# Kernel tuning notes

Hardware: AMD Instinct MI355X
Metric: run time of the kernel (lower is better)

The kernel has to match this reference:

```python
import jax, jax.numpy as jnp
import numpy as np

EPS = 1e-6
NEG = -1e9
W = 8          # chunk_size
H_MA = 4       # monotonic heads
H_CA = 1       # chunkwise heads
ADIM = 1024
SHARP = 1.0    # sharpening_factor
SCALE = float(np.sqrt(ADIM))


def moving_sum(x, back, forward):
    # windowed sum over last axis, window = back+forward+1 (small, fixed)
    K = x.shape[-1]
    pad = [(0, 0)] * (x.ndim - 1) + [(back, forward)]
    xp = jnp.pad(x, pad)
    out = xp[..., 0:K]
    for d in range(1, back + forward + 1):
        out = out + xp[..., d:d + K]
    return out


def exclusive_cumsum(x):
    z = jnp.zeros(x.shape[:-1] + (1,), x.dtype)
    return jnp.cumsum(jnp.concatenate([z, x[..., :-1]], axis=-1), axis=-1)


def setup_inputs():
    key0 = jax.random.key(0)
    ks = jax.random.split(key0, 12)
    B, K, Q, D = 16, 2000, 256, 1024
    nrm = lambda k, shp, s=1.0: jax.random.normal(k, shp, jnp.float32) * s
    aw_prev = jnp.zeros((B, H_MA, 1, K), jnp.float32).at[..., 0].set(1.0)
    return {
        'key': nrm(ks[0], (B, K, D)),
        'value': nrm(ks[1], (B, K, D)),
        'query': nrm(ks[2], (B, Q, D)),
        'mask': jnp.ones((B, Q, K), jnp.int32),
        'aw_prev': aw_prev,
        'Wk_ma': nrm(ks[3], (D, ADIM), 0.02), 'bk_ma': jnp.zeros((ADIM,), jnp.float32),
        'Wq_ma': nrm(ks[4], (D, ADIM), 0.02), 'bq_ma': jnp.zeros((ADIM,), jnp.float32),
        'r': jnp.full((1,), -4.0, jnp.float32),
        'Wk_ca': nrm(ks[5], (D, ADIM), 0.02), 'bk_ca': jnp.zeros((ADIM,), jnp.float32),
        'Wq_ca': nrm(ks[6], (D, ADIM), 0.02), 'bq_ca': jnp.zeros((ADIM,), jnp.float32),
        'Wv': nrm(ks[7], (D, ADIM), 0.02), 'bv': jnp.zeros((ADIM,), jnp.float32),
        'Wo': nrm(ks[8], (ADIM, D), 0.02), 'bo': jnp.zeros((D,), jnp.float32),
    }


def reference(key, value, query, mask, aw_prev,
              Wk_ma, bk_ma, Wq_ma, bq_ma, r,
              Wk_ca, bk_ca, Wq_ca, bq_ca, Wv, bv, Wo, bo):
    B, K, D = key.shape
    Q = query.shape[1]
    dk_ma = ADIM // H_MA
    H_tot = H_MA * H_CA
    dk_ca = ADIM // H_tot
    m = (mask[:, None] != 0)  # [B,1,Q,K]

    # ---- monotonic energy: [B,H_ma,Q,K]
    k_ma = (key @ Wk_ma + bk_ma).reshape(B, K, H_MA, dk_ma)
    q_ma = (query @ Wq_ma + bq_ma).reshape(B, Q, H_MA, dk_ma)
    e_ma = jnp.einsum('bqhd,bkhd->bhqk', q_ma, k_ma) / SCALE + r[0]
    e_ma = jnp.where(m, e_ma, NEG)

    # ---- monotonic alignment alpha (parallel training mode)
    p = jax.nn.sigmoid(e_ma)                                  # [B,H,Q,K]
    log1mp = jnp.log(jnp.clip(1.0 - p, EPS, 1.0))
    cp = jnp.exp(exclusive_cumsum(log1mp))                    # safe_cumprod(1-p)

    def step(aw, pc):
        p_i, cp_i = pc                                        # [B,H,K]
        denom = jnp.clip(cp_i, EPS, 1.0)
        aw_new = p_i * cp_i * jnp.cumsum(aw / denom, axis=-1)
        return aw_new, aw_new

    xs = (p.transpose(2, 0, 1, 3), cp.transpose(2, 0, 1, 3))  # [Q,B,H,K]
    _, alphas = jax.lax.scan(step, aw_prev[:, :, 0], xs)
    alpha = alphas.transpose(1, 2, 0, 3)                      # [B,H_ma,Q,K]

    # ---- chunk energy: [B,H_ma*H_ca,Q,K]
    k_ca = (key @ Wk_ca + bk_ca).reshape(B, K, H_tot, dk_ca)
    q_ca = (query @ Wq_ca + bq_ca).reshape(B, Q, H_tot, dk_ca)
    e_ca = jnp.einsum('bqhd,bkhd->bhqk', q_ca, k_ca) / SCALE
    e_ca = jnp.where(m, e_ca, NEG)

    # ---- soft chunkwise attention (moving-sum windowed softmax)
    u = e_ca.reshape(B, H_MA, H_CA, Q, K)
    a5 = alpha[:, :, None] * SHARP                            # [B,H_ma,1,Q,K]
    u = u - jnp.max(u, axis=-1, keepdims=True)
    se = jnp.clip(jnp.exp(u), 1e-5, None)
    denom = moving_sum(se, W - 1, 0)
    beta = se * moving_sum(a5 / denom, 0, W - 1)
    beta = beta.reshape(B, H_tot, Q, K)

    # ---- context + output projection
    v = (value @ Wv + bv).reshape(B, K, H_tot, dk_ca)
    cv = jnp.einsum('bhqk,bkhd->bqhd', beta, v).reshape(B, Q, ADIM)
    return cv @ Wo + bo
```

## Files before the change

### kernel.cpp

```cpp
#include <hip/hip_runtime.h>


typedef __bf16 bf16x8_t __attribute__((ext_vector_type(8)));
typedef float f32x4_t __attribute__((ext_vector_type(4)));
typedef unsigned short ushort8_t __attribute__((ext_vector_type(8)));
typedef unsigned short ushort4_t __attribute__((ext_vector_type(4)));
typedef unsigned int uint4_t __attribute__((ext_vector_type(4)));

__device__ __forceinline__ unsigned short f2bf(float x) {
  unsigned int u = __builtin_bit_cast(unsigned int, x);
  u += 0x7fffu + ((u >> 16) & 1u);
  return (unsigned short)(u >> 16);
}
__device__ __forceinline__ float bf2f(unsigned short h) {
  unsigned int u = ((unsigned int)h) << 16;
  return __builtin_bit_cast(float, u);
}

__device__ __forceinline__ void gld16(const unsigned short* g, unsigned short* l) {
  __builtin_amdgcn_global_load_lds(
      (const __attribute__((address_space(1))) void*)g,
      (__attribute__((address_space(3))) void*)l, 16, 0, 0);
}

__device__ __forceinline__ float wave_incl_scan(float x) {
  float v = x;
  int mv;
#define DPP_ADD(ctrl, rmask, bctrl)                                           \
  mv = __builtin_amdgcn_update_dpp(0, __builtin_bit_cast(int, v), ctrl,       \
                                   rmask, 0xf, bctrl);                        \
  v += __builtin_bit_cast(float, mv);
  DPP_ADD(0x111, 0xf, true);
  DPP_ADD(0x112, 0xf, true);
  DPP_ADD(0x114, 0xf, true);
  DPP_ADD(0x118, 0xf, true);
  DPP_ADD(0x142, 0xa, false);
  DPP_ADD(0x143, 0xc, false);
#undef DPP_ADD
  return v;
}

__device__ __forceinline__ float wave_max_bcast(float x) {
  const float NI = -__builtin_inff();
  float v = x;
  int mv;
#define DPP_MAX(ctrl, rmask)                                                  \
  mv = __builtin_amdgcn_update_dpp(__builtin_bit_cast(int, NI),               \
                                   __builtin_bit_cast(int, v), ctrl, rmask,   \
                                   0xf, false);                               \
  v = fmaxf(v, __builtin_bit_cast(float, mv));
  DPP_MAX(0x111, 0xf) DPP_MAX(0x112, 0xf) DPP_MAX(0x114, 0xf)
  DPP_MAX(0x118, 0xf) DPP_MAX(0x142, 0xa) DPP_MAX(0x143, 0xc)
#undef DPP_MAX
  int r = __builtin_amdgcn_readlane(__builtin_bit_cast(int, v), 63);
  return __builtin_bit_cast(float, r);
}

#define WSHR1(dst, src)                                                       \
  {                                                                           \
    int _t = __builtin_amdgcn_update_dpp(0, __builtin_bit_cast(int, src),     \
                                         0x138, 0xf, 0xf, true);              \
    dst = __builtin_bit_cast(float, _t);                                      \
  }
#define WSHL1(dst, src)                                                       \
  {                                                                           \
    int _t = __builtin_amdgcn_update_dpp(0, __builtin_bit_cast(int, src),     \
                                         0x130, 0xf, 0xf, true);              \
    dst = __builtin_bit_cast(float, _t);                                      \
  }

__device__ __forceinline__ void gemm_bt_tile(
    const unsigned short* __restrict__ A, long lda,
    const unsigned short* __restrict__ B, long ldb,
    int Kd, unsigned short* lA, unsigned short* lB, f32x4_t acc[4][4]) {
  const int tid = threadIdx.x;
  const int lane = tid & 63;
  const int wid = tid >> 6;
  const int wm = wid >> 1, wn = wid & 1;
  const int lr = lane & 15, quad = lane >> 4;
  const int srow = wid * 32 + (lane >> 3);
  const int scol = ((lane & 7) ^ (lane >> 3)) * 8;
  const int rs = lr & 7;
  for (int ks = 0; ks < Kd; ks += 64) {
    __syncthreads();
    const unsigned short* Ag = A + (long)srow * lda + ks + scol;
    const unsigned short* Bg = B + (long)srow * ldb + ks + scol;
#pragma unroll
    for (int r = 0; r < 4; ++r) {
      gld16(Ag + (long)(r * 8) * lda, lA + (wid * 32 + r * 8) * 64);
      gld16(Bg + (long)(r * 8) * ldb, lB + (wid * 32 + r * 8) * 64);
    }
    __syncthreads();
#pragma unroll
    for (int kk = 0; kk < 2; ++kk) {
      bf16x8_t afr[4], bfr[4];
#pragma unroll
      for (int i = 0; i < 4; ++i)
        afr[i] = *(const bf16x8_t*)(lA + (wm * 64 + i * 16 + lr) * 64 +
                                    (((kk * 4 + quad) ^ rs) << 3));
#pragma unroll
      for (int j = 0; j < 4; ++j)
        bfr[j] = *(const bf16x8_t*)(lB + (wn * 64 + j * 16 + lr) * 64 +
                                    (((kk * 4 + quad) ^ rs) << 3));
#pragma unroll
      for (int i = 0; i < 4; ++i)
#pragma unroll
        for (int j = 0; j < 4; ++j)
          acc[i][j] = __builtin_amdgcn_mfma_f32_16x16x32_bf16(afr[i], bfr[j], acc[i][j], 0, 0, 0);
    }
  }
}

#define EPILOGUE_IDX()                                          \
  const int tid = threadIdx.x, lane = tid & 63, wid = tid >> 6; \
  const int wm = wid >> 1, wn = wid & 1, lr = lane & 15, quad = lane >> 4;

#define ACC_INIT()                              \
  f32x4_t acc[4][4];                            \
  _Pragma("unroll") for (int i = 0; i < 4; ++i) \
  _Pragma("unroll") for (int j = 0; j < 4; ++j) \
  _Pragma("unroll") for (int r = 0; r < 4; ++r) acc[i][j][r] = 0.f;

__device__ __forceinline__ void epi_stash(float* lT, f32x4_t (&acc)[4][4],
                                          int i, int wm, int wn, int lr, int quad) {
#pragma unroll
  for (int j = 0; j < 4; ++j) {
    int lcol = wn * 64 + j * 16 + lr;
#pragma unroll
    for (int r = 0; r < 4; ++r) {
      int lrow = wm * 16 + quad * 4 + r;
      lT[lrow * 128 + (((lcol >> 2) ^ (lrow & 7)) << 2) + (lcol & 3)] = acc[i][j][r];
    }
  }
}
__device__ __forceinline__ f32x4_t epi_read(const float* lT, int rloc, int col4) {
  return *(const f32x4_t*)&lT[rloc * 128 + ((col4 ^ (rloc & 7)) << 2)];
}

__global__ __launch_bounds__(256) void k_proj(const unsigned short* __restrict__ A,
                                              const unsigned short* __restrict__ Wt,
                                              const float* __restrict__ bias,
                                              unsigned short* __restrict__ C) {
  __shared__ __attribute__((aligned(16))) char smem[32768];
  unsigned short* lA = (unsigned short*)smem;
  unsigned short* lB = (unsigned short*)(smem + 16384);
  float* lT = (float*)smem;
  ACC_INIT();
  int flat = blockIdx.x;
  int mb = (flat >> 6) * 8 + (flat & 7);
  int nb = (flat >> 3) & 7;
  const unsigned short* Ab = A + (long)mb * 128 * 1024;
  const unsigned short* Bb = Wt + (long)nb * 128 * 1024;
  gemm_bt_tile(Ab, 1024, Bb, 1024, 1024, lA, lB, acc);
  EPILOGUE_IDX();
  (void)lane;
  long mbase = (long)mb * 128;
  int nbase = nb * 128;
  const int rloc = tid >> 3, c7 = tid & 7;
#pragma unroll
  for (int i = 0; i < 4; ++i) {
    __syncthreads();
    epi_stash(lT, acc, i, wm, wn, lr, quad);
    __syncthreads();
    long mg = mbase + (rloc >> 4) * 64 + i * 16 + (rloc & 15);
    unsigned short* crow = C + mg * 1024 + nbase;
    const float* brow = bias + nbase;
#pragma unroll
    for (int m = 0; m < 4; ++m) {
      int col4 = c7 + 8 * m;
      f32x4_t v = epi_read(lT, rloc, col4);
      f32x4_t bv = *(const f32x4_t*)&brow[col4 * 4];
      ushort4_t o;
#pragma unroll
      for (int z = 0; z < 4; ++z) o[z] = f2bf(v[z] + bv[z]);
      *(ushort4_t*)(crow + col4 * 4) = o;
    }
  }
}

__global__ __launch_bounds__(256) void k_maskpack(const int* __restrict__ mask,
                                                  unsigned int* __restrict__ mw) {
  int lane = threadIdx.x & 63, wid = threadIdx.x >> 6;
  int row = blockIdx.x * 4 + wid;
  const int* mp = mask + (long)row * 2000;
  unsigned int* op = mw + (long)row * 64;
  for (int c = 0; c < 32; ++c) {
    int k = c * 64 + lane;
    int v = (k < 2000) ? mp[k] : 0;
    unsigned long long b = __ballot(v != 0);
    if (lane == 0) {
      op[c * 2] = (unsigned int)b;
      op[c * 2 + 1] = (unsigned int)(b >> 32);
    }
  }
}

__global__ __launch_bounds__(256) void k_escore(const unsigned short* __restrict__ qproj,
                                                const unsigned short* __restrict__ kproj,
                                                const unsigned int* __restrict__ maskw,
                                                const float* __restrict__ rptr,
                                                unsigned short* __restrict__ outp, int is_ma) {
  __shared__ __attribute__((aligned(16))) char smem[32768];
  unsigned short* lA = (unsigned short*)smem;
  unsigned short* lB = (unsigned short*)(smem + 16384);
  float* lT = (float*)smem;
  ACC_INIT();
  int bz = blockIdx.z, b = bz >> 2, h = bz & 3;
  int nrow0 = blockIdx.x * 128;
  const unsigned short* Ab = qproj + ((long)b * 256 + blockIdx.y * 128) * 1024 + h * 256;
  const unsigned short* Bb = kproj + ((long)b * 2048 + nrow0) * 1024 + h * 256;
  gemm_bt_tile(Ab, 1024, Bb, 1024, 256, lA, lB, acc);
  float rv = is_ma ? rptr[0] : 0.f;
  EPILOGUE_IDX();
  (void)lane;
  const int rloc = tid >> 3, c7 = tid & 7;
#pragma unroll
  for (int i = 0; i < 4; ++i) {
    __syncthreads();
    epi_stash(lT, acc, i, wm, wn, lr, quad);
    __syncthreads();
    int qg = blockIdx.y * 128 + (rloc >> 4) * 64 + i * 16 + (rloc & 15);
    uint4_t mw4 = *(const uint4_t*)(maskw + (((long)b * 256 + qg) << 6) + (nrow0 >> 5));
    unsigned short* orow = outp + ((long)bz * 256 + qg) * 2048 + nrow0;
#pragma unroll
    for (int m = 0; m < 4; ++m) {
      int col4 = c7 + 8 * m;
      f32x4_t v = epi_read(lT, rloc, col4);
      unsigned int bits = (mw4[m] >> (4 * c7)) & 0xFu;
      ushort4_t o;
#pragma unroll
      for (int z = 0; z < 4; ++z) {
        float e = v[z] * 0.03125f;
        bool valid = (bits >> z) & 1u;
        float ov;
        if (is_ma)
          ov = valid ? (1.f / (1.f + __expf(-(e + rv)))) : 0.f;
        else
          ov = valid ? e : -1e9f;
        o[z] = f2bf(ov);
      }
      *(ushort4_t*)(orow + col4 * 4) = o;
    }
  }
}

__global__ __launch_bounds__(256) void k_cp(const unsigned short* __restrict__ p,
                                            unsigned short* __restrict__ cp) {
  __shared__ float wsum[4];
  long base = (long)blockIdx.x * 2048;
  int tid = threadIdx.x, lane = tid & 63, wid = tid >> 6;
  ushort8_t p8 = *(const ushort8_t*)(p + base + tid * 8);
  float lex[8], s1 = 0.f;
#pragma unroll
  for (int i = 0; i < 8; ++i) {
    float om = fminf(fmaxf(1.f - bf2f((unsigned short)p8[i]), 1e-6f), 1.f);
    lex[i] = s1;
    s1 += __logf(om);
  }
  float incl = wave_incl_scan(s1);
  if (lane == 63) wsum[wid] = incl;
  __syncthreads();
  float off = incl - s1;
  if (wid > 0) off += wsum[0];
  if (wid > 1) off += wsum[1];
  if (wid > 2) off += wsum[2];
  ushort8_t o;
#pragma unroll
  for (int i = 0; i < 8; ++i) o[i] = f2bf(__expf(off + lex[i]));
  *(ushort8_t*)(cp + base + tid * 8) = o;
}

__global__ __launch_bounds__(256) void k_scan(const unsigned short* __restrict__ p,
                                              const unsigned short* cp,
                                              const float* __restrict__ awp,
                                              unsigned short* alpha) {
  __shared__ unsigned short lsp[2][2][2048];
  __shared__ unsigned short lsc[2][2][2048];
  __shared__ float wsum[2][4];
  int bh = blockIdx.x;
  int tid = threadIdx.x, lane = tid & 63, w = tid >> 6;
  long base = (long)bh * 256 * 2048;
  float aw[8];
  const float* ap = awp + (long)bh * 2000;
#pragma unroll
  for (int i = 0; i < 8; ++i) {
    int k = tid * 8 + i;
    aw[i] = (k < 2000) ? ap[k] : 0.f;
  }
  const unsigned short* pg = p + base;
  const unsigned short* cg = cp + base;
  unsigned short* ag = alpha + base;
  const int sa = w >> 1;
  const int sr = w & 1;
  const unsigned short* sbase = (sa ? cg : pg) + (long)sr * 2048 + lane * 8;
#define STAGE(c, b)                                                           \
  {                                                                           \
    const unsigned short* _src = sbase + (long)(c) * 2 * 2048;                \
    unsigned short* _dst = sa ? &lsc[b][sr][0] : &lsp[b][sr][0];              \
    _Pragma("unroll") for (int _q = 0; _q < 4; ++_q)                          \
        gld16(_src + _q * 512, _dst + _q * 512);                              \
  }
  STAGE(0, 0);
  asm volatile("s_waitcnt vmcnt(0)" ::: "memory");
  __builtin_amdgcn_s_barrier();
  asm volatile("" ::: "memory");
  for (int c = 0; c < 128; ++c) {
    const int b = c & 1;
    if (c < 127) STAGE(c + 1, b ^ 1);
#pragma unroll
    for (int cr = 0; cr < 2; ++cr) {
      const int q = c * 2 + cr;
      ushort8_t p8 = *(const ushort8_t*)&lsp[b][cr][tid * 8];
      ushort8_t c8 = *(const ushort8_t*)&lsc[b][cr][tid * 8];
      float pc[8], rd[8];
#pragma unroll
      for (int i = 0; i < 8; ++i) {
        float pv = bf2f((unsigned short)p8[i]);
        float cv = bf2f((unsigned short)c8[i]);
        pc[i] = pv * cv;
        rd[i] = __builtin_amdgcn_rcpf(fminf(fmaxf(cv, 1e-6f), 1.f));
      }
      float t[8], s1 = 0.f;
#pragma unroll
      for (int i = 0; i < 8; ++i) {
        s1 = fmaf(aw[i], rd[i], s1);
        t[i] = s1;
      }
      float incl = wave_incl_scan(s1);
      if (lane == 63) wsum[q & 1][w] = incl;
      asm volatile("s_waitcnt lgkmcnt(0)" ::: "memory");
      __builtin_amdgcn_s_barrier();
      asm volatile("" ::: "memory");
      float off = incl - s1;
      if (w > 0) off += wsum[q & 1][0];
      if (w > 1) off += wsum[q & 1][1];
      if (w > 2) off += wsum[q & 1][2];
      ushort8_t o;
#pragma unroll
      for (int i = 0; i < 8; ++i) {
        aw[i] = pc[i] * (t[i] + off);
        o[i] = f2bf(aw[i]);
      }
      *(ushort8_t*)(ag + (long)q * 2048 + tid * 8) = o;
    }
    asm volatile("s_waitcnt vmcnt(2)" ::: "memory");
    __builtin_amdgcn_s_barrier();
    asm volatile("" ::: "memory");
  }
#undef STAGE
}

__global__ __launch_bounds__(256) void k_beta(unsigned short* eca,
                                              const unsigned short* __restrict__ alpha) {
  __shared__ float red[4];
  __shared__ float edgeB[4][8];
  __shared__ float edgeF[4][8];
  long base = (long)blockIdx.x * 2048 + threadIdx.x * 8;
  int tid = threadIdx.x, lane = tid & 63, wid = tid >> 6;
  (void)tid;
  ushort8_t u8 = *(const ushort8_t*)(eca + base);
  ushort8_t a8 = *(const ushort8_t*)(alpha + base);
  float u[8], a[8];
#pragma unroll
  for (int i = 0; i < 8; ++i) {
    u[i] = bf2f((unsigned short)u8[i]);
    a[i] = bf2f((unsigned short)a8[i]);
  }
  float m = u[0];
#pragma unroll
  for (int i = 1; i < 8; ++i) m = fmaxf(m, u[i]);
  m = wave_max_bcast(m);
  if (lane == 0) red[wid] = m;
  __syncthreads();
  m = fmaxf(fmaxf(red[0], red[1]), fmaxf(red[2], red[3]));
  float se[8], lp[8];
  float s = 0.f;
#pragma unroll
  for (int i = 0; i < 8; ++i) {
    se[i] = fmaxf(__expf(u[i] - m), 1e-5f);
    s += se[i];
    lp[i] = s;
  }
  float plp[8];
#pragma unroll
  for (int i = 0; i < 8; ++i) WSHR1(plp[i], lp[i]);
  if (lane == 63) {
#pragma unroll
    for (int i = 0; i < 8; ++i) edgeB[wid][i] = lp[i];
  }
  __syncthreads();
  if (lane == 0 && wid > 0) {
#pragma unroll
    for (int i = 0; i < 8; ++i) plp[i] = edgeB[wid - 1][i];
  }
  float sra[8], lf[8];
  s = 0.f;
#pragma unroll
  for (int i = 0; i < 8; ++i) {
    float msb = lp[i] + plp[7] - plp[i];
    sra[i] = a[i] * __builtin_amdgcn_rcpf(msb);
    s += sra[i];
    lf[i] = s;
  }
  float nlf[8];
#pragma unroll
  for (int i = 0; i < 8; ++i) WSHL1(nlf[i], lf[i]);
  if (lane == 0) {
#pragma unroll
    for (int i = 0; i < 8; ++i) edgeF[wid][i] = lf[i];
  }
  __syncthreads();
  if (lane == 63 && wid < 3) {
#pragma unroll
    for (int i = 0; i < 8; ++i) nlf[i] = edgeF[wid + 1][i];
  }
  ushort8_t o;
#pragma unroll
  for (int i = 0; i < 8; ++i) {
    float own = lf[7] - (i ? lf[i - 1] : 0.f);
    float nxt = i ? nlf[i - 1] : 0.f;
    o[i] = f2bf(se[i] * (own + nxt));
  }
  *(ushort8_t*)(eca + base) = o;
}

__global__ __launch_bounds__(256) void k_build_vT(const unsigned short* __restrict__ v,
                                                  unsigned short* __restrict__ vT) {
  __shared__ unsigned short t[64][68];
  int bz = blockIdx.z, b = bz >> 2, h = bz & 3;
  int k0 = blockIdx.x * 64, d0 = blockIdx.y * 64;
  int tx = threadIdx.x & 63, tg = threadIdx.x >> 6;
#pragma unroll
  for (int i = 0; i < 16; ++i) {
    int kk = tg * 16 + i;
    t[kk][tx] = v[((long)(b * 2048 + k0 + kk)) * 1024 + h * 256 + d0 + tx];
  }
  __syncthreads();
#pragma unroll
  for (int i = 0; i < 16; ++i) {
    int dd = tg * 16 + i;
    vT[((long)bz * 256 + d0 + dd) * 2048 + k0 + tx] = t[tx][dd];
  }
}

__global__ __launch_bounds__(256) void k_cv(const unsigned short* __restrict__ beta,
                                            const unsigned short* __restrict__ vT,
                                            unsigned short* __restrict__ cv) {
  __shared__ __attribute__((aligned(16))) char smem[32768];
  unsigned short* lA = (unsigned short*)smem;
  unsigned short* lB = (unsigned short*)(smem + 16384);
  float* lT = (float*)smem;
  ACC_INIT();
  int bz = blockIdx.z, b = bz >> 2, h = bz & 3;
  const unsigned short* Ab = beta + (long)bz * 256 * 2048 + (long)blockIdx.y * 128 * 2048;
  const unsigned short* Bb = vT + (long)bz * 256 * 2048 + (long)blockIdx.x * 128 * 2048;
  gemm_bt_tile(Ab, 2048, Bb, 2048, 2048, lA, lB, acc);
  EPILOGUE_IDX();
  (void)lane;
  const int rloc = tid >> 3, c7 = tid & 7;
#pragma unroll
  for (int i = 0; i < 4; ++i) {
    __syncthreads();
    epi_stash(lT, acc, i, wm, wn, lr, quad);
    __syncthreads();
    long mg = (long)b * 256 + blockIdx.y * 128 + (rloc >> 4) * 64 + i * 16 + (rloc & 15);
    unsigned short* crow = cv + mg * 1024 + h * 256 + blockIdx.x * 128;
#pragma unroll
    for (int m = 0; m < 4; ++m) {
      int col4 = c7 + 8 * m;
      f32x4_t v = epi_read(lT, rloc, col4);
      ushort4_t o;
#pragma unroll
      for (int z = 0; z < 4; ++z) o[z] = f2bf(v[z]);
      *(ushort4_t*)(crow + col4 * 4) = o;
    }
  }
}

__global__ __launch_bounds__(256) void k_out(const unsigned short* __restrict__ cv,
                                             const unsigned short* __restrict__ WoT,
                                             const float* __restrict__ bo,
                                             float* __restrict__ outp) {
  __shared__ __attribute__((aligned(16))) char smem[32768];
  unsigned short* lA = (unsigned short*)smem;
  unsigned short* lB = (unsigned short*)(smem + 16384);
  float* lT = (float*)smem;
  ACC_INIT();
  const unsigned short* Ab = cv + (long)blockIdx.y * 128 * 1024;
  const unsigned short* Bb = WoT + (long)blockIdx.x * 128 * 1024;
  gemm_bt_tile(Ab, 1024, Bb, 1024, 1024, lA, lB, acc);
  EPILOGUE_IDX();
  (void)lane;
  const int rloc = tid >> 3, c7 = tid & 7;
#pragma unroll
  for (int i = 0; i < 4; ++i) {
    __syncthreads();
    epi_stash(lT, acc, i, wm, wn, lr, quad);
    __syncthreads();
    long mg = (long)blockIdx.y * 128 + (rloc >> 4) * 64 + i * 16 + (rloc & 15);
    float* orow = outp + mg * 1024 + blockIdx.x * 128;
    const float* brow = bo + blockIdx.x * 128;
#pragma unroll
    for (int m = 0; m < 4; ++m) {
      int col4 = c7 + 8 * m;
      f32x4_t v = epi_read(lT, rloc, col4);
      f32x4_t bv = *(const f32x4_t*)&brow[col4 * 4];
      *(f32x4_t*)&orow[col4 * 4] = v + bv;
    }
  }
}

__global__ __launch_bounds__(256) void k_twT(const float* __restrict__ W,
                                             unsigned short* __restrict__ Wt) {
  __shared__ float t[32][33];
  int bx = blockIdx.x, by = blockIdx.y;
  int lx = threadIdx.x & 31, ly = threadIdx.x >> 5;
#pragma unroll
  for (int r = 0; r < 4; ++r)
    t[ly + 8 * r][lx] = W[((long)(by * 32 + ly + 8 * r)) * 1024 + bx * 32 + lx];
  __syncthreads();
#pragma unroll
  for (int r = 0; r < 4; ++r)
    Wt[((long)(bx * 32 + ly + 8 * r)) * 1024 + by * 32 + lx] = f2bf(t[lx][ly + 8 * r]);
}

__global__ __launch_bounds__(256) void k_cvt_pad(const float* __restrict__ src,
                                                 unsigned short* __restrict__ dst) {
  long idx = (long)blockIdx.x * 256 + threadIdx.x;
  int b = (int)(idx >> 18);
  int rem = (int)(idx & 262143);
  int row = rem >> 7;
  int c8 = rem & 127;
  ushort8_t o;
  if (row < 2000) {
    const float* sp = src + ((long)(b * 2000 + row)) * 1024 + c8 * 8;
    float4 f0 = *(const float4*)sp;
    float4 f1 = *(const float4*)(sp + 4);
    o[0] = f2bf(f0.x); o[1] = f2bf(f0.y); o[2] = f2bf(f0.z); o[3] = f2bf(f0.w);
    o[4] = f2bf(f1.x); o[5] = f2bf(f1.y); o[6] = f2bf(f1.z); o[7] = f2bf(f1.w);
  } else {
#pragma unroll
    for (int z = 0; z < 8; ++z) o[z] = 0;
  }
  *(ushort8_t*)(dst + idx * 8) = o;
}

__global__ __launch_bounds__(256) void k_cvt(const float* __restrict__ src,
                                             unsigned short* __restrict__ dst) {
  long idx = (long)blockIdx.x * 256 + threadIdx.x;
  const float* sp = src + idx * 8;
  float4 f0 = *(const float4*)sp;
  float4 f1 = *(const float4*)(sp + 4);
  ushort8_t o;
  o[0] = f2bf(f0.x); o[1] = f2bf(f0.y); o[2] = f2bf(f0.z); o[3] = f2bf(f0.w);
  o[4] = f2bf(f1.x); o[5] = f2bf(f1.y); o[6] = f2bf(f1.z); o[7] = f2bf(f1.w);
  *(ushort8_t*)(dst + idx * 8) = o;
}

extern "C" void kernel_launch(void* const* d_in, const int* in_sizes, int n_in,
                              void* d_out, int out_size, void* d_ws, size_t ws_size,
                              hipStream_t stream) {
  const float* key = (const float*)d_in[0];
  const float* value = (const float*)d_in[1];
  const float* query = (const float*)d_in[2];
  const int* mask = (const int*)d_in[3];
  const float* awp = (const float*)d_in[4];
  const float* Wk_ma = (const float*)d_in[5];
  const float* bk_ma = (const float*)d_in[6];
  const float* Wq_ma = (const float*)d_in[7];
  const float* bq_ma = (const float*)d_in[8];
  const float* rvec = (const float*)d_in[9];
  const float* Wk_ca = (const float*)d_in[10];
  const float* bk_ca = (const float*)d_in[11];
  const float* Wq_ca = (const float*)d_in[12];
  const float* bq_ca = (const float*)d_in[13];
  const float* Wv = (const float*)d_in[14];
  const float* bv = (const float*)d_in[15];
  const float* Wo = (const float*)d_in[16];
  const float* bo = (const float*)d_in[17];
  float* outp = (float*)d_out;
  (void)in_sizes; (void)n_in; (void)out_size;

  char* ws = (char*)d_ws;
  size_t off = 0;
  auto alloc = [&](size_t bytes) {
    void* pp = ws + off;
    off += (bytes + 255) & ~(size_t)255;
    return pp;
  };
  unsigned short* wt[6];
  for (int i = 0; i < 6; ++i) wt[i] = (unsigned short*)alloc(1024L * 1024 * 2);
  unsigned short* xbf = (unsigned short*)alloc(16L * 2048 * 1024 * 2);
  unsigned short* qbf = (unsigned short*)alloc(4096L * 1024 * 2);
  unsigned short* kproj = (unsigned short*)alloc(16L * 2048 * 1024 * 2);
  unsigned short* qproj = (unsigned short*)alloc(4096L * 1024 * 2);
  unsigned short* bufP = (unsigned short*)alloc(64L * 256 * 2048 * 2);
  unsigned short* bufA = (unsigned short*)alloc(64L * 256 * 2048 * 2);
  unsigned int* maskw = (unsigned int*)alloc(4096L * 64 * 4);
  if (ws_size < off) return;
  unsigned short* cv_bf = qbf;

  dim3 blk(256);
  k_twT<<<dim3(32, 32), blk, 0, stream>>>(Wk_ma, wt[0]);
  k_twT<<<dim3(32, 32), blk, 0, stream>>>(Wq_ma, wt[1]);
  k_twT<<<dim3(32, 32), blk, 0, stream>>>(Wk_ca, wt[2]);
  k_twT<<<dim3(32, 32), blk, 0, stream>>>(Wq_ca, wt[3]);
  k_twT<<<dim3(32, 32), blk, 0, stream>>>(Wv, wt[4]);
  k_twT<<<dim3(32, 32), blk, 0, stream>>>(Wo, wt[5]);
  k_maskpack<<<dim3(1024), blk, 0, stream>>>(mask, maskw);
  k_cvt_pad<<<dim3(16384), blk, 0, stream>>>(key, xbf);
  k_cvt<<<dim3(2048), blk, 0, stream>>>(query, qbf);
  k_proj<<<dim3(2048), blk, 0, stream>>>(xbf, wt[0], bk_ma, kproj);
  k_proj<<<dim3(256), blk, 0, stream>>>(qbf, wt[1], bq_ma, qproj);
  k_escore<<<dim3(16, 2, 64), blk, 0, stream>>>(qproj, kproj, maskw, rvec, bufP, 1);
  k_cp<<<dim3(16384), blk, 0, stream>>>(bufP, bufA);
  k_proj<<<dim3(2048), blk, 0, stream>>>(xbf, wt[2], bk_ca, kproj);
  k_proj<<<dim3(256), blk, 0, stream>>>(qbf, wt[3], bq_ca, qproj);
  k_scan<<<dim3(64), blk, 0, stream>>>(bufP, bufA, awp, bufA);
  k_escore<<<dim3(16, 2, 64), blk, 0, stream>>>(qproj, kproj, maskw, rvec, bufP, 0);
  k_beta<<<dim3(16384), blk, 0, stream>>>(bufP, bufA);
  k_cvt_pad<<<dim3(16384), blk, 0, stream>>>(value, xbf);
  k_proj<<<dim3(2048), blk, 0, stream>>>(xbf, wt[4], bv, kproj);
  k_build_vT<<<dim3(32, 4, 64), blk, 0, stream>>>(kproj, bufA);
  k_cv<<<dim3(2, 2, 64), blk, 0, stream>>>(bufP, bufA, cv_bf);
  k_out<<<dim3(8, 32), blk, 0, stream>>>(cv_bf, wt[5], bo, outp);
}
```

Measured before the change: 1.031 ms.

## Double-buffer GEMM LDS tiles and triple-buffer monotonic scan staging

The shared GEMM tile loop now uses two LDS buffers per operand, issuing the global-to-LDS loads for the next K step before computing on the current one, with explicit vmcnt waits and raw barriers in place of the two syncthreads per step. The monotonic alpha scan kernel moves from two to three staging buffers so loads run two chunks ahead. The aim is to hide global load latency behind MFMA and scan work. The cost is doubled GEMM shared memory (64KB per block), which may lower occupancy, plus reliance on hand-tuned vmcnt counts being correct.

```diff
diff --git a/kernel.cpp b/kernel.cpp
--- a/kernel.cpp
+++ b/kernel.cpp
@@ -69,10 +69,22 @@
     dst = __builtin_bit_cast(float, _t);                                      \
   }
 
+__device__ __forceinline__ void gemm_stage(const unsigned short* Ag, long lda,
+                                           const unsigned short* Bg, long ldb,
+                                           int wid, unsigned short* lA,
+                                           unsigned short* lB) {
+#pragma unroll
+  for (int r = 0; r < 4; ++r) {
+    gld16(Ag + (long)(r * 8) * lda, lA + (wid * 32 + r * 8) * 64);
+    gld16(Bg + (long)(r * 8) * ldb, lB + (wid * 32 + r * 8) * 64);
+  }
+}
+
 __device__ __forceinline__ void gemm_bt_tile(
     const unsigned short* __restrict__ A, long lda,
-    const unsigned short* __restrict__ B, long ldb,
-    int Kd, unsigned short* lA, unsigned short* lB, f32x4_t acc[4][4]) {
+    const unsigned short* __restrict__ B, long ldb, int Kd,
+    unsigned short* lA0, unsigned short* lB0,
+    unsigned short* lA1, unsigned short* lB1, f32x4_t acc[4][4]) {
   const int tid = threadIdx.x;
   const int lane = tid & 63;
   const int wid = tid >> 6;
@@ -81,26 +93,33 @@
   const int srow = wid * 32 + (lane >> 3);
   const int scol = ((lane & 7) ^ (lane >> 3)) * 8;
   const int rs = lr & 7;
-  for (int ks = 0; ks < Kd; ks += 64) {
-    __syncthreads();
-    const unsigned short* Ag = A + (long)srow * lda + ks + scol;
-    const unsigned short* Bg = B + (long)srow * ldb + ks + scol;
-#pragma unroll
-    for (int r = 0; r < 4; ++r) {
-      gld16(Ag + (long)(r * 8) * lda, lA + (wid * 32 + r * 8) * 64);
-      gld16(Bg + (long)(r * 8) * ldb, lB + (wid * 32 + r * 8) * 64);
-    }
-    __syncthreads();
+  const unsigned short* Ag = A + (long)srow * lda + scol;
+  const unsigned short* Bg = B + (long)srow * ldb + scol;
+  const int nt = Kd >> 6;
+  gemm_stage(Ag, lda, Bg, ldb, wid, lA0, lB0);
+  for (int t = 0; t < nt; ++t) {
+    unsigned short* cA = (t & 1) ? lA1 : lA0;
+    unsigned short* cB = (t & 1) ? lB1 : lB0;
+    if (t + 1 < nt) {
+      unsigned short* nA = (t & 1) ? lA0 : lA1;
+      unsigned short* nB = (t & 1) ? lB0 : lB1;
+      gemm_stage(Ag + (t + 1) * 64, lda, Bg + (t + 1) * 64, ldb, wid, nA, nB);
+      asm volatile("s_waitcnt vmcnt(8)" ::: "memory");
+    } else {
+      asm volatile("s_waitcnt vmcnt(0)" ::: "memory");
+    }
+    __builtin_amdgcn_s_barrier();
+    asm volatile("" ::: "memory");
 #pragma unroll
     for (int kk = 0; kk < 2; ++kk) {
       bf16x8_t afr[4], bfr[4];
 #pragma unroll
       for (int i = 0; i < 4; ++i)
-        afr[i] = *(const bf16x8_t*)(lA + (wm * 64 + i * 16 + lr) * 64 +
+        afr[i] = *(const bf16x8_t*)(cA + (wm * 64 + i * 16 + lr) * 64 +
                                     (((kk * 4 + quad) ^ rs) << 3));
 #pragma unroll
       for (int j = 0; j < 4; ++j)
-        bfr[j] = *(const bf16x8_t*)(lB + (wn * 64 + j * 16 + lr) * 64 +
+        bfr[j] = *(const bf16x8_t*)(cB + (wn * 64 + j * 16 + lr) * 64 +
                                     (((kk * 4 + quad) ^ rs) << 3));
 #pragma unroll
       for (int i = 0; i < 4; ++i)
@@ -108,6 +127,8 @@
         for (int j = 0; j < 4; ++j)
           acc[i][j] = __builtin_amdgcn_mfma_f32_16x16x32_bf16(afr[i], bfr[j], acc[i][j], 0, 0, 0);
     }
+    asm volatile("" ::: "memory");
+    __builtin_amdgcn_s_barrier();
   }
 }
 
@@ -121,6 +142,14 @@
   _Pragma("unroll") for (int j = 0; j < 4; ++j) \
   _Pragma("unroll") for (int r = 0; r < 4; ++r) acc[i][j][r] = 0.f;
 
+#define GEMM_SMEM()                                        \
+  __shared__ __attribute__((aligned(16))) char smem[65536]; \
+  unsigned short* lA0 = (unsigned short*)smem;             \
+  unsigned short* lB0 = (unsigned short*)(smem + 16384);   \
+  unsigned short* lA1 = (unsigned short*)(smem + 32768);   \
+  unsigned short* lB1 = (unsigned short*)(smem + 49152);   \
+  float* lT = (float*)smem;
+
 __device__ __forceinline__ void epi_stash(float* lT, f32x4_t (&acc)[4][4],
                                           int i, int wm, int wn, int lr, int quad) {
 #pragma unroll
@@ -141,17 +170,14 @@
                                               const unsigned short* __restrict__ Wt,
                                               const float* __restrict__ bias,
                                               unsigned short* __restrict__ C) {
-  __shared__ __attribute__((aligned(16))) char smem[32768];
-  unsigned short* lA = (unsigned short*)smem;
-  unsigned short* lB = (unsigned short*)(smem + 16384);
-  float* lT = (float*)smem;
+  GEMM_SMEM();
   ACC_INIT();
   int flat = blockIdx.x;
   int mb = (flat >> 6) * 8 + (flat & 7);
   int nb = (flat >> 3) & 7;
   const unsigned short* Ab = A + (long)mb * 128 * 1024;
   const unsigned short* Bb = Wt + (long)nb * 128 * 1024;
-  gemm_bt_tile(Ab, 1024, Bb, 1024, 1024, lA, lB, acc);
+  gemm_bt_tile(Ab, 1024, Bb, 1024, 1024, lA0, lB0, lA1, lB1, acc);
   EPILOGUE_IDX();
   (void)lane;
   long mbase = (long)mb * 128;
@@ -200,16 +226,13 @@
                                                 const unsigned int* __restrict__ maskw,
                                                 const float* __restrict__ rptr,
                                                 unsigned short* __restrict__ outp, int is_ma) {
-  __shared__ __attribute__((aligned(16))) char smem[32768];
-  unsigned short* lA = (unsigned short*)smem;
-  unsigned short* lB = (unsigned short*)(smem + 16384);
-  float* lT = (float*)smem;
+  GEMM_SMEM();
   ACC_INIT();
   int bz = blockIdx.z, b = bz >> 2, h = bz & 3;
   int nrow0 = blockIdx.x * 128;
   const unsigned short* Ab = qproj + ((long)b * 256 + blockIdx.y * 128) * 1024 + h * 256;
   const unsigned short* Bb = kproj + ((long)b * 2048 + nrow0) * 1024 + h * 256;
-  gemm_bt_tile(Ab, 1024, Bb, 1024, 256, lA, lB, acc);
+  gemm_bt_tile(Ab, 1024, Bb, 1024, 256, lA0, lB0, lA1, lB1, acc);
   float rv = is_ma ? rptr[0] : 0.f;
   EPILOGUE_IDX();
   (void)lane;
@@ -274,8 +297,8 @@
                                               const unsigned short* cp,
                                               const float* __restrict__ awp,
                                               unsigned short* alpha) {
-  __shared__ unsigned short lsp[2][2][2048];
-  __shared__ unsigned short lsc[2][2][2048];
+  __shared__ unsigned short lsp[3][2][2048];
+  __shared__ unsigned short lsc[3][2][2048];
   __shared__ float wsum[2][4];
   int bh = blockIdx.x;
   int tid = threadIdx.x, lane = tid & 63, w = tid >> 6;
@@ -301,12 +324,19 @@
         gld16(_src + _q * 512, _dst + _q * 512);                              \
   }
   STAGE(0, 0);
-  asm volatile("s_waitcnt vmcnt(0)" ::: "memory");
-  __builtin_amdgcn_s_barrier();
-  asm volatile("" ::: "memory");
+  STAGE(1, 1);
   for (int c = 0; c < 128; ++c) {
-    const int b = c & 1;
-    if (c < 127) STAGE(c + 1, b ^ 1);
+    const int b = c % 3;
+    if (c + 2 < 128) {
+      STAGE(c + 2, (c + 2) % 3);
+      asm volatile("s_waitcnt vmcnt(8)" ::: "memory");
+    } else if (c + 1 < 128) {
+      asm volatile("s_waitcnt vmcnt(4)" ::: "memory");
+    } else {
+      asm volatile("s_waitcnt vmcnt(0)" ::: "memory");
+    }
+    __builtin_amdgcn_s_barrier();
+    asm volatile("" ::: "memory");
 #pragma unroll
     for (int cr = 0; cr < 2; ++cr) {
       const int q = c * 2 + cr;
@@ -343,9 +373,6 @@
       }
       *(ushort8_t*)(ag + (long)q * 2048 + tid * 8) = o;
     }
-    asm volatile("s_waitcnt vmcnt(2)" ::: "memory");
-    __builtin_amdgcn_s_barrier();
-    asm volatile("" ::: "memory");
   }
 #undef STAGE
 }
@@ -446,15 +473,12 @@
 __global__ __launch_bounds__(256) void k_cv(const unsigned short* __restrict__ beta,
                                             const unsigned short* __restrict__ vT,
                                             unsigned short* __restrict__ cv) {
-  __shared__ __attribute__((aligned(16))) char smem[32768];
-  unsigned short* lA = (unsigned short*)smem;
-  unsigned short* lB = (unsigned short*)(smem + 16384);
-  float* lT = (float*)smem;
+  GEMM_SMEM();
   ACC_INIT();
   int bz = blockIdx.z, b = bz >> 2, h = bz & 3;
   const unsigned short* Ab = beta + (long)bz * 256 * 2048 + (long)blockIdx.y * 128 * 2048;
   const unsigned short* Bb = vT + (long)bz * 256 * 2048 + (long)blockIdx.x * 128 * 2048;
-  gemm_bt_tile(Ab, 2048, Bb, 2048, 2048, lA, lB, acc);
+  gemm_bt_tile(Ab, 2048, Bb, 2048, 2048, lA0, lB0, lA1, lB1, acc);
   EPILOGUE_IDX();
   (void)lane;
   const int rloc = tid >> 3, c7 = tid & 7;
@@ -481,14 +505,11 @@
                                              const unsigned short* __restrict__ WoT,
                                              const float* __restrict__ bo,
                                              float* __restrict__ outp) {
-  __shared__ __attribute__((aligned(16))) char smem[32768];
-  unsigned short* lA = (unsigned short*)smem;
-  unsigned short* lB = (unsigned short*)(smem + 16384);
-  float* lT = (float*)smem;
+  GEMM_SMEM();
   ACC_INIT();
   const unsigned short* Ab = cv + (long)blockIdx.y * 128 * 1024;
   const unsigned short* Bb = WoT + (long)blockIdx.x * 128 * 1024;
-  gemm_bt_tile(Ab, 1024, Bb, 1024, 1024, lA, lB, acc);
+  gemm_bt_tile(Ab, 1024, Bb, 1024, 1024, lA0, lB0, lA1, lB1, acc);
   EPILOGUE_IDX();
   (void)lane;
   const int rloc = tid >> 3, c7 = tid & 7;
```

Result: faster. 1.009 ms (-2.2%).
